# Performance work log

Measured on AMD Instinct MI355X. Metric: run time of the kernel, lower is better.

## Reference

```python
import jax, jax.numpy as jnp
import numpy as np

C = 1024
H = 16
EPS = 1e-5

def _layernorm(x, g, b):
    mu = jnp.mean(x, axis=-1, keepdims=True)
    var = jnp.mean(jnp.square(x - mu), axis=-1, keepdims=True)
    return (x - mu) * jax.lax.rsqrt(var + EPS) * g + b

def _mha(xq, xkv, wq, bq, wk, bk, wv, bv, wo, bo, causal):
    B, T, Cm = xq.shape
    Tc = xkv.shape[1]
    d = Cm // H
    q = (xq @ wq + bq).reshape(B, T, H, d)
    k = (xkv @ wk + bk).reshape(B, Tc, H, d)
    v = (xkv @ wv + bv).reshape(B, Tc, H, d)
    att = jnp.einsum('bthd,bshd->bhts', q, k) * (1.0 / np.sqrt(d))
    if causal:
        mask = jnp.tril(jnp.ones((T, Tc), dtype=bool))
        att = jnp.where(mask[None, None], att, -jnp.inf)
    att = jax.nn.softmax(att, axis=-1)
    y = jnp.einsum('bhts,bshd->bthd', att, v).reshape(B, T, Cm)
    return y @ wo + bo


def setup_inputs() -> dict:
    key = jax.random.key(0)
    ks = jax.random.split(key, 20)
    s = 0.02
    w = lambda k: (s * jax.random.normal(k, (C, C))).astype(jnp.float32)
    inp = {
        'x': jax.random.normal(ks[0], (4, 1024, C), dtype=jnp.float32),
        'context': jax.random.normal(ks[1], (4, 1024, C), dtype=jnp.float32),
        'ln1_g': jnp.ones((C,)), 'ln1_b': jnp.zeros((C,)),
        'ln2_g': jnp.ones((C,)), 'ln2_b': jnp.zeros((C,)),
        'sa_wq': w(ks[2]), 'sa_bq': jnp.zeros((C,)),
        'sa_wk': w(ks[3]), 'sa_bk': jnp.zeros((C,)),
        'sa_wv': w(ks[4]), 'sa_bv': jnp.zeros((C,)),
        'sa_wo': w(ks[5]), 'sa_bo': jnp.zeros((C,)),
        'ca_wq': w(ks[6]), 'ca_bq': jnp.zeros((C,)),
        'ca_wk': w(ks[7]), 'ca_bk': jnp.zeros((C,)),
        'ca_wv': w(ks[8]), 'ca_bv': jnp.zeros((C,)),
        'ca_wo': w(ks[9]), 'ca_bo': jnp.zeros((C,)),
        'mlp_w1': (s * jax.random.normal(ks[10], (C, 4 * C))).astype(jnp.float32),
        'mlp_b1': jnp.zeros((4 * C,)),
        'mlp_w2': (s * jax.random.normal(ks[11], (4 * C, C))).astype(jnp.float32),
        'mlp_b2': jnp.zeros((C,)),
    }
    return inp


def reference(x, context, ln1_g, ln1_b, ln2_g, ln2_b,
              sa_wq, sa_bq, sa_wk, sa_bk, sa_wv, sa_bv, sa_wo, sa_bo,
              ca_wq, ca_bq, ca_wk, ca_bk, ca_wv, ca_bv, ca_wo, ca_bo,
              mlp_w1, mlp_b1, mlp_w2, mlp_b2):
    # x = x + self_attn(ln1(x))  (causal)
    x = x + _mha(_layernorm(x, ln1_g, ln1_b), _layernorm(x, ln1_g, ln1_b),
                 sa_wq, sa_bq, sa_wk, sa_bk, sa_wv, sa_bv, sa_wo, sa_bo, causal=True)
    # x = x + cross_attn(ln2(x), context)  (non-causal)
    x = x + _mha(_layernorm(x, ln2_g, ln2_b), context,
                 ca_wq, ca_bq, ca_wk, ca_bk, ca_wv, ca_bv, ca_wo, ca_bo, causal=False)
    # x = x + mlp(ln2(x))  -- note: the module reuses ln2 here (as in source)
    h = _layernorm(x, ln2_g, ln2_b)
    h = jax.nn.gelu(h @ mlp_w1 + mlp_b1, approximate=False) @ mlp_w2 + mlp_b2
    x = x + h
    return x
```

## Files before the change

kernel.cpp:

```cpp
#include <hip/hip_runtime.h>
#include <hip/hip_bf16.h>

typedef __attribute__((ext_vector_type(8))) short s8v;
typedef __attribute__((ext_vector_type(4))) float f4v;

#define DEV static __device__ __forceinline__

DEV unsigned short f2bf(float f) {
    unsigned int u = __builtin_bit_cast(unsigned int, f);
    unsigned int r = u + 0x7FFFu + ((u >> 16) & 1u);
    return (unsigned short)(r >> 16);
}

DEV f4v fzero() { f4v v = {0.f, 0.f, 0.f, 0.f}; return v; }

DEV float fgelu(float x) {
    float z = x * (1.5957691f + 0.07135482f * x * x);
    float s = __builtin_amdgcn_rcpf(1.0f + __expf(-z));
    return x * s;
}

DEV void gload16(const void* g, void* l) {
    __builtin_amdgcn_global_load_lds(
        (const __attribute__((address_space(1))) unsigned int*)g,
        (__attribute__((address_space(3))) unsigned int*)l, 16, 0, 0);
}

struct P8 { const float* p[8]; };
__global__ __launch_bounds__(256) void k_transpose8(
        P8 ws8, unsigned short* __restrict__ base) {
    __shared__ float tile[32][33];
    int z = blockIdx.z;
    const float* W = ws8.p[z];
    unsigned short* Wt = base + (size_t)z * 1024 * 1024;
    int tx = threadIdx.x & 31, ty = threadIdx.x >> 5;
    int n0 = blockIdx.x * 32, k0 = blockIdx.y * 32;
#pragma unroll
    for (int r = 0; r < 32; r += 8)
        tile[ty + r][tx] = W[(size_t)(k0 + ty + r) * 1024 + n0 + tx];
    __syncthreads();
#pragma unroll
    for (int r = 0; r < 32; r += 8)
        Wt[(size_t)(n0 + ty + r) * 1024 + k0 + tx] = f2bf(tile[tx][ty + r]);
}

__global__ __launch_bounds__(256) void k_transpose_bf16(
        const float* __restrict__ W, unsigned short* __restrict__ Wt, int K, int N) {
    __shared__ float tile[32][33];
    int tx = threadIdx.x & 31, ty = threadIdx.x >> 5;
    int n0 = blockIdx.x * 32, k0 = blockIdx.y * 32;
#pragma unroll
    for (int r = 0; r < 32; r += 8)
        tile[ty + r][tx] = W[(size_t)(k0 + ty + r) * N + n0 + tx];
    __syncthreads();
#pragma unroll
    for (int r = 0; r < 32; r += 8)
        Wt[(size_t)(n0 + ty + r) * K + k0 + tx] = f2bf(tile[tx][ty + r]);
}

__global__ __launch_bounds__(256) void k_f32_to_bf16(
        const float* __restrict__ in, unsigned short* __restrict__ out, int n) {
    int i = (blockIdx.x * 256 + threadIdx.x) * 8;
    if (i >= n) return;
    float4 a = *(const float4*)(in + i);
    float4 b = *(const float4*)(in + i + 4);
    uint4 o;
    o.x = f2bf(a.x) | ((unsigned)f2bf(a.y) << 16);
    o.y = f2bf(a.z) | ((unsigned)f2bf(a.w) << 16);
    o.z = f2bf(b.x) | ((unsigned)f2bf(b.y) << 16);
    o.w = f2bf(b.z) | ((unsigned)f2bf(b.w) << 16);
    *(uint4*)(out + i) = o;
}

__global__ __launch_bounds__(256) void k_bias_cat(
        const float* q, const float* k, const float* v,
        const float* k2, const float* v2, float* out) {
    int i = blockIdx.x * 256 + threadIdx.x;
    float val;
    if (i < 1024) val = q[i];
    else if (i < 2048) val = k[i - 1024];
    else if (i < 3072) val = v[i - 2048];
    else if (i < 4096) val = k2[i - 3072];
    else val = v2[i - 4096];
    out[i] = val;
}

__global__ __launch_bounds__(256) void k_layernorm(
        const float* __restrict__ x, const float* __restrict__ g,
        const float* __restrict__ b, unsigned short* __restrict__ out) {
    int row = blockIdx.x;
    int t = threadIdx.x;
    const float* xr = x + (size_t)row * 1024;
    float4 v = *(const float4*)(xr + t * 4);
    float s = v.x + v.y + v.z + v.w;
    float ss = v.x * v.x + v.y * v.y + v.z * v.z + v.w * v.w;
#pragma unroll
    for (int m = 1; m < 64; m <<= 1) { s += __shfl_xor(s, m); ss += __shfl_xor(ss, m); }
    __shared__ float red[16];
    int w = t >> 6;
    if ((t & 63) == 0) { red[w] = s; red[8 + w] = ss; }
    __syncthreads();
    s = red[0] + red[1] + red[2] + red[3];
    ss = red[8] + red[9] + red[10] + red[11];
    float mu = s * (1.f / 1024.f);
    float rstd = rsqrtf(ss * (1.f / 1024.f) - mu * mu + 1e-5f);
    float4 gv = *(const float4*)(g + t * 4);
    float4 bv = *(const float4*)(b + t * 4);
    float y0 = (v.x - mu) * rstd * gv.x + bv.x;
    float y1 = (v.y - mu) * rstd * gv.y + bv.y;
    float y2 = (v.z - mu) * rstd * gv.z + bv.z;
    float y3 = (v.w - mu) * rstd * gv.w + bv.w;
    uint2 o;
    o.x = f2bf(y0) | ((unsigned)f2bf(y1) << 16);
    o.y = f2bf(y2) | ((unsigned)f2bf(y3) << 16);
    *(uint2*)(out + (size_t)row * 1024 + t * 4) = o;
}

template <int EPI, int BM>
__global__ __launch_bounds__(256) void k_gemm(
        const unsigned short* __restrict__ A, const unsigned short* __restrict__ Bt,
        const float* __restrict__ bias, const float* __restrict__ res,
        void* __restrict__ outv, int M, int N, int K) {
    constexpr int WI = (BM == 128) ? 4 : 2;
    constexpr int ABUF = BM * 64;
    constexpr int BUFSZ = ABUF + 8192;
    __shared__ __align__(16) char smem[3 * BUFSZ];
    int nbx = N >> 7;
    int bid = blockIdx.x;
    int cpx = gridDim.x >> 3;
    int swz = (bid & 7) * cpx + (bid >> 3);
    int bx = swz % nbx, by = swz / nbx;
    int m0 = by * BM, n0 = bx << 7;
    int tid = threadIdx.x, w = tid >> 6, l = tid & 63;
    int wr = w >> 1, wc = w & 1;
    int lq = l >> 4, lc = l & 15;
    f4v acc[WI][4];
#pragma unroll
    for (int i = 0; i < WI; ++i)
#pragma unroll
        for (int j = 0; j < 4; ++j) acc[i][j] = fzero();
    const unsigned short* Ab = A + (size_t)m0 * K;
    const unsigned short* Bb = Bt + (size_t)n0 * K;
    int arow = w * 16 + (l >> 2);
    int ach = (((l & 3) ^ ((arow >> 1) & 3)) << 3);

    auto STAGE = [&](int t) {
        int kt = t << 5;
        char* buf = smem + (t % 3) * BUFSZ;
        gload16(Ab + (size_t)arow * K + kt + ach, buf + w * 1024);
        if constexpr (BM == 128)
            gload16(Ab + (size_t)(64 + arow) * K + kt + ach, buf + 4096 + w * 1024);
        gload16(Bb + (size_t)arow * K + kt + ach, buf + ABUF + w * 1024);
        gload16(Bb + (size_t)(64 + arow) * K + kt + ach, buf + ABUF + 4096 + w * 1024);
    };
    int cs = ((lq ^ ((lc >> 1) & 3)) << 4);
    auto COMPUTE = [&](int t) {
        const char* buf = smem + (t % 3) * BUFSZ;
        s8v af[WI], bfr[4];
#pragma unroll
        for (int i = 0; i < WI; ++i)
            af[i] = *(const s8v*)(buf + (wr * (BM / 2) + i * 16 + lc) * 64 + cs);
#pragma unroll
        for (int j = 0; j < 4; ++j)
            bfr[j] = *(const s8v*)(buf + ABUF + (wc * 64 + j * 16 + lc) * 64 + cs);
#pragma unroll
        for (int i = 0; i < WI; ++i)
#pragma unroll
            for (int j = 0; j < 4; ++j)
                acc[i][j] = __builtin_amdgcn_mfma_f32_16x16x32_bf16(af[i], bfr[j], acc[i][j], 0, 0, 0);
    };

    int NT = K >> 5;
    STAGE(0); STAGE(1);
    if constexpr (BM == 128) asm volatile("s_waitcnt vmcnt(4)" ::: "memory");
    else                     asm volatile("s_waitcnt vmcnt(3)" ::: "memory");
    __builtin_amdgcn_s_barrier();
    for (int t = 0; t < NT; ++t) {
        if (t + 2 < NT) STAGE(t + 2);
        COMPUTE(t);
        if (t + 2 < NT) {
            if constexpr (BM == 128) asm volatile("s_waitcnt vmcnt(4)" ::: "memory");
            else                     asm volatile("s_waitcnt vmcnt(3)" ::: "memory");
        } else if (t + 1 < NT) {
            asm volatile("s_waitcnt vmcnt(0)" ::: "memory");
        }
        __builtin_amdgcn_s_barrier();
    }

    float* esc = (float*)smem + w * 1088;
#pragma unroll
    for (int i = 0; i < WI; ++i) {
#pragma unroll
        for (int j = 0; j < 4; ++j)
#pragma unroll
            for (int r = 0; r < 4; ++r)
                esc[(lq * 4 + r) * 68 + j * 16 + lc] = acc[i][j][r];
#pragma unroll
        for (int p = 0; p < 4; ++p) {
            int rr = p * 4 + lq;
            float4 v = *(const float4*)(esc + rr * 68 + lc * 4);
            int row = m0 + wr * (BM / 2) + i * 16 + rr;
            int col = n0 + wc * 64 + lc * 4;
            float4 bv = *(const float4*)(bias + col);
            v.x += bv.x; v.y += bv.y; v.z += bv.z; v.w += bv.w;
            size_t idx = (size_t)row * N + col;
            if (EPI == 0) {
                ushort4 o;
                o.x = f2bf(v.x); o.y = f2bf(v.y); o.z = f2bf(v.z); o.w = f2bf(v.w);
                *(ushort4*)((unsigned short*)outv + idx) = o;
            } else if (EPI == 1) {
                ushort4 o;
                o.x = f2bf(fgelu(v.x)); o.y = f2bf(fgelu(v.y));
                o.z = f2bf(fgelu(v.z)); o.w = f2bf(fgelu(v.w));
                *(ushort4*)((unsigned short*)outv + idx) = o;
            } else {
                float4 rv = *(const float4*)(res + idx);
                v.x += rv.x; v.y += rv.y; v.z += rv.z; v.w += rv.w;
                *(float4*)((float*)outv + idx) = v;
            }
        }
    }
}

template <int EPI>
__global__ __launch_bounds__(256, 2) void k_gemm2(
        const unsigned short* __restrict__ A, const unsigned short* __restrict__ Bt,
        const float* __restrict__ bias, void* __restrict__ outv,
        int M, int N, int K) {
    constexpr int BUFSZ = 8192 + 16384;
    __shared__ __align__(16) char smem[3 * BUFSZ];
    int nbx = N >> 8;
    int bid = blockIdx.x;
    int cpx = gridDim.x >> 3;
    int swz = (bid & 7) * cpx + (bid >> 3);
    int bx = swz % nbx, by = swz / nbx;
    int m0 = by << 7, n0 = bx << 8;
    int tid = threadIdx.x, w = tid >> 6, l = tid & 63;
    int wr = w >> 1, wc = w & 1;
    int lq = l >> 4, lc = l & 15;
    f4v acc[4][8];
#pragma unroll
    for (int i = 0; i < 4; ++i)
#pragma unroll
        for (int j = 0; j < 8; ++j) acc[i][j] = fzero();
    const unsigned short* Ab = A + (size_t)m0 * K;
    const unsigned short* Bb = Bt + (size_t)n0 * K;
    int arow = w * 16 + (l >> 2);
    int ach = (((l & 3) ^ ((arow >> 1) & 3)) << 3);

    auto STAGE = [&](int t) {
        int kt = t << 5;
        char* buf = smem + (t % 3) * BUFSZ;
        gload16(Ab + (size_t)arow * K + kt + ach, buf + w * 1024);
        gload16(Ab + (size_t)(64 + arow) * K + kt + ach, buf + 4096 + w * 1024);
#pragma unroll
        for (int h = 0; h < 4; ++h)
            gload16(Bb + (size_t)(h * 64 + arow) * K + kt + ach,
                    buf + 8192 + h * 4096 + w * 1024);
    };
    int cs = ((lq ^ ((lc >> 1) & 3)) << 4);
    auto COMPUTE = [&](int t) {
        const char* buf = smem + (t % 3) * BUFSZ;
        s8v af[4], bfr[8];
#pragma unroll
        for (int i = 0; i < 4; ++i)
            af[i] = *(const s8v*)(buf + (wr * 64 + i * 16 + lc) * 64 + cs);
#pragma unroll
        for (int j = 0; j < 8; ++j)
            bfr[j] = *(const s8v*)(buf + 8192 + (wc * 128 + j * 16 + lc) * 64 + cs);
#pragma unroll
        for (int i = 0; i < 4; ++i)
#pragma unroll
            for (int j = 0; j < 8; ++j)
                acc[i][j] = __builtin_amdgcn_mfma_f32_16x16x32_bf16(af[i], bfr[j], acc[i][j], 0, 0, 0);
    };

    int NT = K >> 5;
    STAGE(0); STAGE(1);
    asm volatile("s_waitcnt vmcnt(6)" ::: "memory");
    __builtin_amdgcn_s_barrier();
    for (int t = 0; t < NT; ++t) {
        if (t + 2 < NT) STAGE(t + 2);
        COMPUTE(t);
        if (t + 2 < NT) {
            asm volatile("s_waitcnt vmcnt(6)" ::: "memory");
        } else if (t + 1 < NT) {
            asm volatile("s_waitcnt vmcnt(0)" ::: "memory");
        }
        __builtin_amdgcn_s_barrier();
    }

    float* esc = (float*)smem + w * 2112;
#pragma unroll
    for (int i = 0; i < 4; ++i) {
#pragma unroll
        for (int j = 0; j < 8; ++j)
#pragma unroll
            for (int r = 0; r < 4; ++r)
                esc[(lq * 4 + r) * 132 + j * 16 + lc] = acc[i][j][r];
#pragma unroll
        for (int p = 0; p < 4; ++p) {
            int rr = p * 4 + lq;
            int row = m0 + wr * 64 + i * 16 + rr;
#pragma unroll
            for (int h = 0; h < 2; ++h) {
                float4 v = *(const float4*)(esc + rr * 132 + h * 64 + lc * 4);
                int col = n0 + wc * 128 + h * 64 + lc * 4;
                float4 bv = *(const float4*)(bias + col);
                v.x += bv.x; v.y += bv.y; v.z += bv.z; v.w += bv.w;
                size_t idx = (size_t)row * N + col;
                ushort4 o;
                if (EPI == 0) {
                    o.x = f2bf(v.x); o.y = f2bf(v.y); o.z = f2bf(v.z); o.w = f2bf(v.w);
                } else {
                    o.x = f2bf(fgelu(v.x)); o.y = f2bf(fgelu(v.y));
                    o.z = f2bf(fgelu(v.z)); o.w = f2bf(fgelu(v.w));
                }
                *(ushort4*)((unsigned short*)outv + idx) = o;
            }
        }
    }
}

template <bool CAUSAL>
__global__ __launch_bounds__(256) void k_attn(
        const unsigned short* __restrict__ Q, int ldq,
        const unsigned short* __restrict__ Kp, int ldk,
        const unsigned short* __restrict__ Vp, int ldv,
        unsigned short* __restrict__ O, int ldo, int T) {
    __shared__ unsigned short Ks[2][64 * 64];
    __shared__ unsigned short Vt[2][64 * 64];
    __shared__ unsigned short Ps[4][16 * 64];
    int nqt = T >> 6;
    int qt0, qt1, bh;
    if (CAUSAL) {
        int pairs = nqt >> 1;
        int pr = blockIdx.x % pairs;
        bh = blockIdx.x / pairs;
        qt0 = pr; qt1 = nqt - 1 - pr;
    } else {
        qt1 = blockIdx.x % nqt;
        bh = blockIdx.x / nqt;
        qt0 = 0;
    }
    int b = bh >> 4, h = bh & 15;
    int tid = threadIdx.x, w = tid >> 6, l = tid & 63;
    int lq = l >> 4, lc = l & 15;
    size_t qoff = (size_t)b * T * ldq + h * 64;
    size_t koff = (size_t)b * T * ldk + h * 64;
    size_t voff = (size_t)b * T * ldv + h * 64;
    s8v qf1[2], qf0[2];
    {
        const unsigned short* qp = Q + qoff + (size_t)(qt1 * 64 + w * 16 + lc) * ldq + lq * 8;
        qf1[0] = *(const s8v*)qp;
        qf1[1] = *(const s8v*)(qp + 32);
        if (CAUSAL) {
            const unsigned short* q0p = Q + qoff + (size_t)(qt0 * 64 + w * 16 + lc) * ldq + lq * 8;
            qf0[0] = *(const s8v*)q0p;
            qf0[1] = *(const s8v*)(q0p + 32);
        }
    }
    s8v ones;
#pragma unroll
    for (int i = 0; i < 8; ++i) ones[i] = (short)0x3F80;
    f4v o1[4], o0[4];
    float l1r[4], l0r[4];
    float m1 = -3.0e38f, m0 = -3.0e38f;
#pragma unroll
    for (int j = 0; j < 4; ++j) {
        o1[j] = fzero(); o0[j] = fzero(); l1r[j] = 0.f; l0r[j] = 0.f;
    }
    int p = tid & 31, dbase = (tid >> 5) * 8;
    s8v v0r, v1r;

    auto STAGE_K = [&](int kt, int bufi) {
#pragma unroll
        for (int s = 0; s < 2; ++s) {
            int idx = s * 256 + w * 64 + l;
            int t = idx >> 3;
            int ch = (idx & 7) ^ (t & 7);
            gload16(Kp + koff + (size_t)(kt * 64 + t) * ldk + ch * 8,
                    (char*)Ks[bufi] + s * 4096 + w * 1024);
        }
    };
    auto LOAD_V = [&](int kt) {
        const unsigned short* vp = Vp + voff + (size_t)(kt * 64 + 2 * p) * ldv + dbase;
        v0r = *(const s8v*)vp;
        v1r = *(const s8v*)(vp + ldv);
    };
    auto WRITE_V = [&](int bufi) {
#pragma unroll
        for (int j = 0; j < 8; ++j) {
            int dd = dbase + j;
            unsigned int val = (unsigned short)v0r[j] | ((unsigned)(unsigned short)v1r[j] << 16);
            *(unsigned int*)((char*)Vt[bufi] + dd * 128 +
                             ((((p >> 2) ^ (dd & 7)) << 4) | ((p & 3) << 2))) = val;
        }
    };

    const float SC = 0.18033688011112042f;

    auto SMPV = [&](f4v (&sa)[4], f4v (&oa)[4], float& mr, float (&lr)[4],
                    int bufi, int qt, int kt) {
        bool diag = CAUSAL && (kt == qt);
        int qloc = w * 16 + lc;
        float pv[16];
        float tm = -3.0e38f;
#pragma unroll
        for (int jn = 0; jn < 4; ++jn)
#pragma unroll
            for (int j = 0; j < 4; ++j) {
                float sv = sa[jn][j] * SC;
                if (diag && (jn * 16 + lq * 4 + j > qloc)) sv = -3.0e38f;
                pv[jn * 4 + j] = sv;
                tm = fmaxf(tm, sv);
            }
        tm = fmaxf(tm, __shfl_xor(tm, 16));
        tm = fmaxf(tm, __shfl_xor(tm, 32));
        float mnew = fmaxf(mr, tm);
        float alpha = exp2f(mr - mnew);
        mr = mnew;
#pragma unroll
        for (int j = 0; j < 4; ++j) {
            float aj = __shfl(alpha, lq * 4 + j);
            lr[j] *= aj;
#pragma unroll
            for (int jn = 0; jn < 4; ++jn) oa[jn][j] *= aj;
        }
#pragma unroll
        for (int jn = 0; jn < 4; ++jn) {
            int chunk = (jn * 2 + (lq >> 1)) ^ (lc & 7);
            char* basep = (char*)Ps[w] + lc * 128 + (chunk << 4) + ((lq & 1) << 3);
            unsigned e01 = f2bf(exp2f(pv[jn * 4 + 0] - mnew)) |
                           ((unsigned)f2bf(exp2f(pv[jn * 4 + 1] - mnew)) << 16);
            unsigned e23 = f2bf(exp2f(pv[jn * 4 + 2] - mnew)) |
                           ((unsigned)f2bf(exp2f(pv[jn * 4 + 3] - mnew)) << 16);
            *(unsigned*)basep = e01;
            *(unsigned*)(basep + 4) = e23;
        }
        s8v pa[2];
#pragma unroll
        for (int kc = 0; kc < 2; ++kc)
            pa[kc] = *(const s8v*)((const char*)Ps[w] + lc * 128 +
                                   (((kc * 4 + lq) ^ (lc & 7)) << 4));
        f4v sone = fzero();
#pragma unroll
        for (int kc = 0; kc < 2; ++kc) {
            sone = __builtin_amdgcn_mfma_f32_16x16x32_bf16(pa[kc], ones, sone, 0, 0, 0);
#pragma unroll
            for (int jn = 0; jn < 4; ++jn) {
                int dd = jn * 16 + lc;
                s8v bf = *(const s8v*)((const char*)Vt[bufi] + dd * 128 +
                                       (((kc * 4 + lq) ^ (dd & 7)) << 4));
                oa[jn] = __builtin_amdgcn_mfma_f32_16x16x32_bf16(pa[kc], bf, oa[jn], 0, 0, 0);
            }
        }
#pragma unroll
        for (int j = 0; j < 4; ++j) lr[j] += sone[j];
    };

    int ktend = CAUSAL ? (qt1 + 1) : nqt;
    STAGE_K(0, 0); LOAD_V(0);
    asm volatile("s_waitcnt vmcnt(0)" ::: "memory");
    WRITE_V(0);
    __syncthreads();
    int buf = 0;
    for (int kt = 0; kt < ktend; ++kt) {
        bool pf = (kt + 1 < ktend);
        if (pf) { STAGE_K(kt + 1, buf ^ 1); LOAD_V(kt + 1); }
        bool do0 = CAUSAL && (kt <= qt0);
        f4v sa1[4], sa0[4];
#pragma unroll
        for (int jn = 0; jn < 4; ++jn) {
            sa1[jn] = fzero(); sa0[jn] = fzero();
            int t = jn * 16 + lc;
#pragma unroll
            for (int kc = 0; kc < 2; ++kc) {
                s8v kf = *(const s8v*)((const char*)Ks[buf] + t * 128 +
                                       (((kc * 4 + lq) ^ (t & 7)) << 4));
                sa1[jn] = __builtin_amdgcn_mfma_f32_16x16x32_bf16(kf, qf1[kc], sa1[jn], 0, 0, 0);
                if (do0)
                    sa0[jn] = __builtin_amdgcn_mfma_f32_16x16x32_bf16(kf, qf0[kc], sa0[jn], 0, 0, 0);
            }
        }
        SMPV(sa1, o1, m1, l1r, buf, qt1, kt);
        if (do0) SMPV(sa0, o0, m0, l0r, buf, qt0, kt);
        if (pf) {
            asm volatile("s_waitcnt vmcnt(0)" ::: "memory");
            WRITE_V(buf ^ 1);
        }
        __syncthreads();
        buf ^= 1;
    }
#pragma unroll
    for (int j = 0; j < 4; ++j) {
        float inv = 1.0f / l1r[j];
        int row = qt1 * 64 + w * 16 + lq * 4 + j;
#pragma unroll
        for (int jn = 0; jn < 4; ++jn)
            O[(size_t)(b * T + row) * ldo + h * 64 + jn * 16 + lc] = f2bf(o1[jn][j] * inv);
    }
    if (CAUSAL) {
#pragma unroll
        for (int j = 0; j < 4; ++j) {
            float inv = 1.0f / l0r[j];
            int row = qt0 * 64 + w * 16 + lq * 4 + j;
#pragma unroll
            for (int jn = 0; jn < 4; ++jn)
                O[(size_t)(b * T + row) * ldo + h * 64 + jn * 16 + lc] = f2bf(o0[jn][j] * inv);
        }
    }
}

extern "C" void kernel_launch(void* const* d_in, const int* in_sizes, int n_in,
                              void* d_out, int out_size, void* d_ws, size_t ws_size,
                              hipStream_t stream) {
    const float* x     = (const float*)d_in[0];
    const float* ctx   = (const float*)d_in[1];
    const float* ln1_g = (const float*)d_in[2];
    const float* ln1_b = (const float*)d_in[3];
    const float* ln2_g = (const float*)d_in[4];
    const float* ln2_b = (const float*)d_in[5];
    const float* sa_wq = (const float*)d_in[6];  const float* sa_bq = (const float*)d_in[7];
    const float* sa_wk = (const float*)d_in[8];  const float* sa_bk = (const float*)d_in[9];
    const float* sa_wv = (const float*)d_in[10]; const float* sa_bv = (const float*)d_in[11];
    const float* sa_wo = (const float*)d_in[12]; const float* sa_bo = (const float*)d_in[13];
    const float* ca_wq = (const float*)d_in[14]; const float* ca_bq = (const float*)d_in[15];
    const float* ca_wk = (const float*)d_in[16]; const float* ca_bk = (const float*)d_in[17];
    const float* ca_wv = (const float*)d_in[18]; const float* ca_bv = (const float*)d_in[19];
    const float* ca_wo = (const float*)d_in[20]; const float* ca_bo = (const float*)d_in[21];
    const float* w1 = (const float*)d_in[22]; const float* b1 = (const float*)d_in[23];
    const float* w2 = (const float*)d_in[24]; const float* b2 = (const float*)d_in[25];
    float* out = (float*)d_out;

    char* ws = (char*)d_ws;
    const size_t MB = 1024 * 1024;
    unsigned short* wt_base = (unsigned short*)(ws + 0 * MB);
    unsigned short* wt_saq = wt_base + 0 * 1024 * 1024;
    unsigned short* wt_cak = wt_base + 5 * 1024 * 1024;
    unsigned short* wt_sao = wt_base + 3 * 1024 * 1024;
    unsigned short* wt_caq = wt_base + 4 * 1024 * 1024;
    unsigned short* wt_cao = wt_base + 7 * 1024 * 1024;
    unsigned short* w1t    = (unsigned short*)(ws + 16 * MB);
    unsigned short* w2t    = (unsigned short*)(ws + 24 * MB);
    unsigned short* ctxb   = (unsigned short*)(ws + 32 * MB);
    float*          x1     = (float*)        (ws + 40 * MB);
    unsigned short* qbuf   = (unsigned short*)(ws + 56 * MB);
    unsigned short* kbuf   = (unsigned short*)(ws + 64 * MB);
    unsigned short* hln    = (unsigned short*)(ws + 80 * MB);
    float*          bcat   = (float*)        (ws + 88 * MB);
    unsigned short* qkv = qbuf;
    unsigned short* kv  = kbuf;
    unsigned short* m1  = qbuf;
    unsigned short* h3  = ctxb;

    dim3 blk(256);
    P8 ws8;
    ws8.p[0] = sa_wq; ws8.p[1] = sa_wk; ws8.p[2] = sa_wv; ws8.p[3] = sa_wo;
    ws8.p[4] = ca_wq; ws8.p[5] = ca_wk; ws8.p[6] = ca_wv; ws8.p[7] = ca_wo;
    k_transpose8<<<dim3(32, 32, 8), blk, 0, stream>>>(ws8, wt_base);
    k_transpose_bf16<<<dim3(128, 32), blk, 0, stream>>>(w1, w1t, 1024, 4096);
    k_transpose_bf16<<<dim3(32, 128), blk, 0, stream>>>(w2, w2t, 4096, 1024);
    k_f32_to_bf16<<<dim3(2048), blk, 0, stream>>>(ctx, ctxb, 4 * 1024 * 1024);
    k_bias_cat<<<dim3(20), blk, 0, stream>>>(sa_bq, sa_bk, sa_bv, ca_bk, ca_bv, bcat);

    k_layernorm<<<dim3(4096), blk, 0, stream>>>(x, ln1_g, ln1_b, hln);
    k_gemm2<0><<<dim3(32 * 12), blk, 0, stream>>>(hln, wt_saq, bcat, qkv, 4096, 3072, 1024);
    k_attn<true><<<dim3(512), blk, 0, stream>>>(qkv, 3072, qkv + 1024, 3072, qkv + 2048, 3072,
                                                hln, 1024, 1024);
    k_gemm<2, 64><<<dim3(64 * 8), blk, 0, stream>>>(hln, wt_sao, sa_bo, x, x1, 4096, 1024, 1024);

    k_layernorm<<<dim3(4096), blk, 0, stream>>>(x1, ln2_g, ln2_b, hln);
    k_gemm<0, 64><<<dim3(64 * 8), blk, 0, stream>>>(hln, wt_caq, ca_bq, nullptr, qbuf, 4096, 1024, 1024);
    k_gemm<0, 128><<<dim3(16 * 32), blk, 0, stream>>>(ctxb, wt_cak, bcat + 3072, nullptr, kv, 4096, 2048, 1024);
    k_attn<false><<<dim3(1024), blk, 0, stream>>>(qbuf, 1024, kv, 2048, kv + 1024, 2048,
                                                  hln, 1024, 1024);
    k_gemm<2, 64><<<dim3(64 * 8), blk, 0, stream>>>(hln, wt_cao, ca_bo, x1, out, 4096, 1024, 1024);

    k_layernorm<<<dim3(4096), blk, 0, stream>>>(out, ln2_g, ln2_b, h3);
    k_gemm2<1><<<dim3(32 * 16), blk, 0, stream>>>(h3, w1t, b1, m1, 4096, 4096, 1024);
    k_gemm<2, 64><<<dim3(64 * 8), blk, 0, stream>>>(m1, w2t, b2, out, out, 4096, 1024, 4096);
}
```

Before: 347.9 us.

## Split GEMM main loop into two phases and raise wave priority around MFMA

The large-tile GEMM main loop is broken into two halves. Each half loads part of the B fragments from LDS, issues half of the next-stage global-to-LDS loads, then runs half of the MFMA block, so memory issue is interleaved with matrix math. s_setprio(1) brackets the MFMA sequences in the GEMMs and in the attention QK and PV loops, favouring the waves that are issuing matrix work. The explicit lgkmcnt waits and sched_barriers pin the instruction order, which could serialize LDS reads and limit the compiler's own scheduling.

```diff
diff --git a/kernel.cpp b/kernel.cpp
--- a/kernel.cpp
+++ b/kernel.cpp
@@ -163,11 +163,13 @@
 #pragma unroll
         for (int j = 0; j < 4; ++j)
             bfr[j] = *(const s8v*)(buf + ABUF + (wc * 64 + j * 16 + lc) * 64 + cs);
+        __builtin_amdgcn_s_setprio(1);
 #pragma unroll
         for (int i = 0; i < WI; ++i)
 #pragma unroll
             for (int j = 0; j < 4; ++j)
                 acc[i][j] = __builtin_amdgcn_mfma_f32_16x16x32_bf16(af[i], bfr[j], acc[i][j], 0, 0, 0);
+        __builtin_amdgcn_s_setprio(0);
     };
 
     int NT = K >> 5;
@@ -248,41 +250,60 @@
     int arow = w * 16 + (l >> 2);
     int ach = (((l & 3) ^ ((arow >> 1) & 3)) << 3);
 
-    auto STAGE = [&](int t) {
+    auto STAGE_P0 = [&](int t) {
         int kt = t << 5;
         char* buf = smem + (t % 3) * BUFSZ;
         gload16(Ab + (size_t)arow * K + kt + ach, buf + w * 1024);
         gload16(Ab + (size_t)(64 + arow) * K + kt + ach, buf + 4096 + w * 1024);
-#pragma unroll
-        for (int h = 0; h < 4; ++h)
-            gload16(Bb + (size_t)(h * 64 + arow) * K + kt + ach,
-                    buf + 8192 + h * 4096 + w * 1024);
+        gload16(Bb + (size_t)arow * K + kt + ach, buf + 8192 + w * 1024);
+        gload16(Bb + (size_t)(64 + arow) * K + kt + ach, buf + 8192 + 4096 + w * 1024);
+    };
+    auto STAGE_P1 = [&](int t) {
+        int kt = t << 5;
+        char* buf = smem + (t % 3) * BUFSZ;
+        gload16(Bb + (size_t)(128 + arow) * K + kt + ach, buf + 8192 + 8192 + w * 1024);
+        gload16(Bb + (size_t)(192 + arow) * K + kt + ach, buf + 8192 + 12288 + w * 1024);
     };
     int cs = ((lq ^ ((lc >> 1) & 3)) << 4);
-    auto COMPUTE = [&](int t) {
-        const char* buf = smem + (t % 3) * BUFSZ;
-        s8v af[4], bfr[8];
-#pragma unroll
-        for (int i = 0; i < 4; ++i)
-            af[i] = *(const s8v*)(buf + (wr * 64 + i * 16 + lc) * 64 + cs);
-#pragma unroll
-        for (int j = 0; j < 8; ++j)
-            bfr[j] = *(const s8v*)(buf + 8192 + (wc * 128 + j * 16 + lc) * 64 + cs);
-#pragma unroll
-        for (int i = 0; i < 4; ++i)
-#pragma unroll
-            for (int j = 0; j < 8; ++j)
-                acc[i][j] = __builtin_amdgcn_mfma_f32_16x16x32_bf16(af[i], bfr[j], acc[i][j], 0, 0, 0);
-    };
 
     int NT = K >> 5;
-    STAGE(0); STAGE(1);
+    STAGE_P0(0); STAGE_P1(0); STAGE_P0(1); STAGE_P1(1);
     asm volatile("s_waitcnt vmcnt(6)" ::: "memory");
     __builtin_amdgcn_s_barrier();
     for (int t = 0; t < NT; ++t) {
-        if (t + 2 < NT) STAGE(t + 2);
-        COMPUTE(t);
-        if (t + 2 < NT) {
+        const char* buf = smem + (t % 3) * BUFSZ;
+        bool pf = (t + 2 < NT);
+        s8v af[4], bfr[8];
+#pragma unroll
+        for (int i = 0; i < 4; ++i)
+            af[i] = *(const s8v*)(buf + (wr * 64 + i * 16 + lc) * 64 + cs);
+#pragma unroll
+        for (int j = 0; j < 4; ++j)
+            bfr[j] = *(const s8v*)(buf + 8192 + (wc * 128 + j * 16 + lc) * 64 + cs);
+        if (pf) STAGE_P0(t + 2);
+        asm volatile("s_waitcnt lgkmcnt(0)" ::: "memory");
+        __builtin_amdgcn_sched_barrier(0);
+        __builtin_amdgcn_s_setprio(1);
+#pragma unroll
+        for (int i = 0; i < 4; ++i)
+#pragma unroll
+            for (int j = 0; j < 4; ++j)
+                acc[i][j] = __builtin_amdgcn_mfma_f32_16x16x32_bf16(af[i], bfr[j], acc[i][j], 0, 0, 0);
+        __builtin_amdgcn_s_setprio(0);
+#pragma unroll
+        for (int j = 4; j < 8; ++j)
+            bfr[j] = *(const s8v*)(buf + 8192 + (wc * 128 + j * 16 + lc) * 64 + cs);
+        if (pf) STAGE_P1(t + 2);
+        asm volatile("s_waitcnt lgkmcnt(0)" ::: "memory");
+        __builtin_amdgcn_sched_barrier(0);
+        __builtin_amdgcn_s_setprio(1);
+#pragma unroll
+        for (int i = 0; i < 4; ++i)
+#pragma unroll
+            for (int j = 4; j < 8; ++j)
+                acc[i][j] = __builtin_amdgcn_mfma_f32_16x16x32_bf16(af[i], bfr[j], acc[i][j], 0, 0, 0);
+        __builtin_amdgcn_s_setprio(0);
+        if (pf) {
             asm volatile("s_waitcnt vmcnt(6)" ::: "memory");
         } else if (t + 1 < NT) {
             asm volatile("s_waitcnt vmcnt(0)" ::: "memory");
@@ -444,6 +465,7 @@
             pa[kc] = *(const s8v*)((const char*)Ps[w] + lc * 128 +
                                    (((kc * 4 + lq) ^ (lc & 7)) << 4));
         f4v sone = fzero();
+        __builtin_amdgcn_s_setprio(1);
 #pragma unroll
         for (int kc = 0; kc < 2; ++kc) {
             sone = __builtin_amdgcn_mfma_f32_16x16x32_bf16(pa[kc], ones, sone, 0, 0, 0);
@@ -455,6 +477,7 @@
                 oa[jn] = __builtin_amdgcn_mfma_f32_16x16x32_bf16(pa[kc], bf, oa[jn], 0, 0, 0);
             }
         }
+        __builtin_amdgcn_s_setprio(0);
 #pragma unroll
         for (int j = 0; j < 4; ++j) lr[j] += sone[j];
     };
@@ -470,6 +493,7 @@
         if (pf) { STAGE_K(kt + 1, buf ^ 1); LOAD_V(kt + 1); }
         bool do0 = CAUSAL && (kt <= qt0);
         f4v sa1[4], sa0[4];
+        __builtin_amdgcn_s_setprio(1);
 #pragma unroll
         for (int jn = 0; jn < 4; ++jn) {
             sa1[jn] = fzero(); sa0[jn] = fzero();
@@ -483,6 +507,7 @@
                     sa0[jn] = __builtin_amdgcn_mfma_f32_16x16x32_bf16(kf, qf0[kc], sa0[jn], 0, 0, 0);
             }
         }
+        __builtin_amdgcn_s_setprio(0);
         SMPV(sa1, o1, m1, l1r, buf, qt1, kt);
         if (do0) SMPV(sa0, o0, m0, l0r, buf, qt0, kt);
         if (pf) {
```

New measurement: 346.3 us. No clear change (-0.5%).
